# Performance work log

Hardware: AMD Instinct MI355X
Metric: run time of the kernel (lower is better)

Reference implementation:

```python
import jax, jax.numpy as jnp
import numpy as np

NUM_HEADS = 16
D_MODEL = 1024
DK = D_MODEL // NUM_HEADS


def setup_inputs() -> dict:
    key = jax.random.key(0)
    kH, kq, kk, kv, ko = jax.random.split(key, 5)
    scale = 0.02
    return {
        "H": jax.random.normal(kH, (4, 2048, D_MODEL), dtype=jnp.float32),
        "Wq": jax.random.normal(kq, (D_MODEL, D_MODEL), dtype=jnp.float32) * scale,
        "Wk": jax.random.normal(kk, (D_MODEL, D_MODEL), dtype=jnp.float32) * scale,
        "Wv": jax.random.normal(kv, (D_MODEL, D_MODEL), dtype=jnp.float32) * scale,
        "Wo": jax.random.normal(ko, (D_MODEL, D_MODEL), dtype=jnp.float32) * scale,
    }


def reference(H, Wq, Wk, Wv, Wo):
    b, T, d = H.shape
    n, dk = NUM_HEADS, DK
    # projections -> [b, n, T, dk]
    def split_heads(x):
        return x.reshape(b, T, n, dk).transpose(0, 2, 1, 3)
    Q = split_heads(H @ Wq)
    K = split_heads(H @ Wk)
    V = split_heads(H @ Wv)
    scores = jnp.einsum("bntd,bnsd->bnts", Q, K) / jnp.sqrt(jnp.float32(dk))
    causal = jnp.tril(jnp.ones((T, T), dtype=bool))
    scores = jnp.where(causal[None, None], scores, -jnp.inf)
    attn = jax.nn.softmax(scores, axis=-1)  # dropout rate 0 -> identity
    out = jnp.einsum("bnts,bnsd->bntd", attn, V)  # [b, n, T, dk]
    out = out.transpose(0, 2, 1, 3).reshape(b, T, n * dk)
    return out @ Wo
```

## Files before the change

### kernel.cpp

```cpp
#include <hip/hip_runtime.h>
#include <hip/hip_bf16.h>

#define T_SEQ 2048
#define DM 1024
#define DM2 2048
#define NH 16
#define DKH 64
#define NBATCH 4
#define MROWS (NBATCH*T_SEQ)

typedef __attribute__((ext_vector_type(8))) short bf16x8;
typedef __attribute__((ext_vector_type(4))) short bf16x4;
typedef __attribute__((ext_vector_type(4))) float f32x4;
typedef __attribute__((ext_vector_type(16))) float f32x16;
typedef __attribute__((ext_vector_type(4))) unsigned short u16x4;

#define NEG_INF (-__builtin_inff())

#if __has_builtin(__builtin_amdgcn_exp2f)
#define EXP2(x) __builtin_amdgcn_exp2f(x)
#else
#define EXP2(x) exp2f(x)
#endif

#define MFMA32(A,B,C) __builtin_amdgcn_mfma_f32_32x32x16_bf16(A,B,C,0,0,0)

static __device__ __forceinline__ unsigned short f2bf(float f){
  union { float f; unsigned u; } v; v.f = f;
  unsigned r = v.u + 0x7fffu + ((v.u >> 16) & 1u);
  return (unsigned short)(r >> 16);
}

static __device__ __forceinline__ unsigned short f2bfc(float f){
  union { __hip_bfloat16 h; unsigned short u; } cv;
  cv.h = __float2bfloat16(f);
  return cv.u;
}

static __device__ __forceinline__ void gload_lds16(const void* g, void* l){
  __builtin_amdgcn_global_load_lds(
      (const __attribute__((address_space(1))) void*)g,
      (__attribute__((address_space(3))) void*)l, 16, 0, 0);
}

__global__ __launch_bounds__(256) void convprep(
    const float* __restrict__ H,
    const float* __restrict__ W0, const float* __restrict__ W1,
    const float* __restrict__ W2, const float* __restrict__ W3,
    u16x4* __restrict__ Hb4,
    unsigned short* __restrict__ O0, unsigned short* __restrict__ O1,
    unsigned short* __restrict__ O2, unsigned short* __restrict__ O3)
{
  __shared__ float t[32][33];
  const int bid = blockIdx.x, tid = threadIdx.x;
  if (bid < 4096){
    const int z = bid >> 10, rem = bid & 1023;
    const int nx = (rem & 31)*32, kx = (rem >> 5)*32;
    const float* W = (z==0)?W0:(z==1)?W1:(z==2)?W2:W3;
    unsigned short* O = (z==0)?O0:(z==1)?O1:(z==2)?O2:O3;
    const float sc = (z==0) ? 0.18033688f : 1.0f;
    const int tx = tid & 31, ty = tid >> 5;
    #pragma unroll
    for (int i = 0; i < 4; ++i)
      t[ty + i*8][tx] = W[(size_t)(kx + ty + i*8)*DM + nx + tx];
    __syncthreads();
    #pragma unroll
    for (int i = 0; i < 4; ++i)
      O[(size_t)(nx + ty + i*8)*DM + kx + tx] = f2bf(t[tx][ty + i*8] * sc);
  } else {
    const int n4 = MROWS*DM/4;
    for (int i = (bid - 4096)*256 + tid; i < n4; i += 2048*256){
      float4 v = ((const float4*)H)[i];
      u16x4 o;
      o[0] = f2bf(v.x); o[1] = f2bf(v.y); o[2] = f2bf(v.z); o[3] = f2bf(v.w);
      Hb4[i] = o;
    }
  }
}

template<bool F32OUT>
static __device__ __forceinline__ void gemm_body(
    const unsigned short* __restrict__ A, const unsigned short* __restrict__ Bt,
    void* __restrict__ Cp, int N, int K, int m0, int n0,
    unsigned short* a_lds, unsigned short* b_lds)
{
  const int tid = threadIdx.x;
  const int w = tid >> 6, l = tid & 63;
  const int g = l >> 4, lr = l & 15;
  const int wr = w >> 1, wc = w & 1;
  f32x4 acc[4][4] = {};
  const int nk = K >> 6;
  for (int ks = 0; ks < nk; ++ks){
    __syncthreads();
    const int k0 = ks << 6;
    #pragma unroll
    for (int i = 0; i < 4; ++i){
      int c = (w*4 + i)*64 + l;
      int row = c >> 3;
      int gc = (c & 7) ^ (row & 7);
      gload_lds16(A + (size_t)(m0 + row)*K + (k0 + gc*8), &a_lds[c*8]);
    }
    #pragma unroll
    for (int i = 0; i < 4; ++i){
      int c = (w*4 + i)*64 + l;
      int row = c >> 3;
      int gc = (c & 7) ^ (row & 7);
      gload_lds16(Bt + (size_t)(n0 + row)*K + (k0 + gc*8), &b_lds[c*8]);
    }
    __syncthreads();
    #pragma unroll
    for (int kc = 0; kc < 2; ++kc){
      bf16x8 af[4], bf_[4];
      #pragma unroll
      for (int mt = 0; mt < 4; ++mt){
        int row = wr*64 + mt*16 + lr;
        int off = row*128 + ((kc*64 + g*16) ^ ((row & 7) << 4));
        af[mt] = *(const bf16x8*)((const char*)a_lds + off);
      }
      #pragma unroll
      for (int nt = 0; nt < 4; ++nt){
        int row = wc*64 + nt*16 + lr;
        int off = row*128 + ((kc*64 + g*16) ^ ((row & 7) << 4));
        bf_[nt] = *(const bf16x8*)((const char*)b_lds + off);
      }
      #pragma unroll
      for (int mt = 0; mt < 4; ++mt)
        #pragma unroll
        for (int nt = 0; nt < 4; ++nt)
          acc[mt][nt] = __builtin_amdgcn_mfma_f32_16x16x32_bf16(af[mt], bf_[nt], acc[mt][nt], 0, 0, 0);
    }
  }
  #pragma unroll
  for (int mt = 0; mt < 4; ++mt){
    #pragma unroll
    for (int nt = 0; nt < 4; ++nt){
      const int col = n0 + wc*64 + nt*16 + lr;
      #pragma unroll
      for (int r = 0; r < 4; ++r){
        const int row = m0 + wr*64 + mt*16 + 4*g + r;
        if (F32OUT) ((float*)Cp)[(size_t)row*N + col] = acc[mt][nt][r];
        else ((unsigned short*)Cp)[(size_t)row*N + col] = f2bf(acc[mt][nt][r]);
      }
    }
  }
}

__global__ __launch_bounds__(256) void gemm_qkv(
    const unsigned short* __restrict__ Hb, const unsigned short* __restrict__ Wqkt,
    unsigned short* __restrict__ QKb,
    const unsigned short* __restrict__ Wvt, unsigned short* __restrict__ Vtb)
{
  __shared__ __attribute__((aligned(16))) unsigned short a_lds[128*64];
  __shared__ __attribute__((aligned(16))) unsigned short b_lds[128*64];
  const int bid = blockIdx.x;
  const unsigned short *A, *Bt; unsigned short* Cp; int N, m0, n0;
  if (bid < 1024){
    A = Hb; Bt = Wqkt; Cp = QKb; N = DM2;
    m0 = (bid & 63)*128; n0 = (bid >> 6)*128;
  } else {
    const int t2 = bid - 1024;
    A = Wvt; Bt = Hb; Cp = Vtb; N = MROWS;
    m0 = (t2 & 7)*128; n0 = (t2 >> 3)*128;
  }
  gemm_body<false>(A, Bt, Cp, N, DM, m0, n0, a_lds, b_lds);
}

__global__ __launch_bounds__(256) void gemm_out(
    const unsigned short* __restrict__ Ab, const unsigned short* __restrict__ Wot,
    float* __restrict__ Out)
{
  __shared__ __attribute__((aligned(16))) unsigned short a_lds[128*64];
  __shared__ __attribute__((aligned(16))) unsigned short b_lds[128*64];
  gemm_body<true>(Ab, Wot, Out, DM, DM, blockIdx.x*128, blockIdx.y*128, a_lds, b_lds);
}

static __device__ __forceinline__ void half_softmax(
    f32x16& st0, f32x16& st1, float& m_run, float& l_run,
    f32x16& acc0, f32x16& acc1, bf16x8 (&pb)[4],
    int kvb, int qg, bool fullT)
{
  if (!fullT){
    #pragma unroll
    for (int r = 0; r < 16; ++r){
      const int kvo = (r & 3) + 4*((r >> 2) & 1) + 16*(r >> 3);
      st0[r] = (kvb + kvo      <= qg) ? st0[r] : NEG_INF;
      st1[r] = (kvb + 32 + kvo <= qg) ? st1[r] : NEG_INF;
    }
  }
  float m01[8];
  #pragma unroll
  for (int r = 0; r < 8; ++r)
    m01[r] = fmaxf(fmaxf(st0[2*r], st0[2*r+1]), fmaxf(st1[2*r], st1[2*r+1]));
  float tm = fmaxf(fmaxf(fmaxf(m01[0],m01[1]), fmaxf(m01[2],m01[3])),
                   fmaxf(fmaxf(m01[4],m01[5]), fmaxf(m01[6],m01[7])));
  float mm = m_run;
  if (!__all(tm - m_run <= 8.f)){
    float tg = fmaxf(tm, __shfl_xor(tm, 32));
    const float mn = fmaxf(m_run, tg);
    const float fac = EXP2(m_run - mn);
    l_run *= fac;
    #pragma unroll
    for (int r = 0; r < 16; ++r){ acc0[r] *= fac; acc1[r] *= fac; }
    m_run = mn; mm = mn;
  }
  float ps0 = 0.f, ps1 = 0.f, ps2 = 0.f, ps3 = 0.f;
  #pragma unroll
  for (int r = 0; r < 4; ++r){
    float e0 = EXP2(st0[4*r+0]-mm), e1 = EXP2(st0[4*r+1]-mm);
    float e2 = EXP2(st0[4*r+2]-mm), e3 = EXP2(st0[4*r+3]-mm);
    float f0 = EXP2(st1[4*r+0]-mm), f1 = EXP2(st1[4*r+1]-mm);
    float f2 = EXP2(st1[4*r+2]-mm), f3 = EXP2(st1[4*r+3]-mm);
    ps0 += e0 + f0; ps1 += e1 + f1; ps2 += e2 + f2; ps3 += e3 + f3;
    st0[4*r+0]=e0; st0[4*r+1]=e1; st0[4*r+2]=e2; st0[4*r+3]=e3;
    st1[4*r+0]=f0; st1[4*r+1]=f1; st1[4*r+2]=f2; st1[4*r+3]=f3;
  }
  l_run += (ps0 + ps1) + (ps2 + ps3);
  #pragma unroll
  for (int m = 0; m < 2; ++m){
    bf16x8 t0, t1;
    #pragma unroll
    for (int i = 0; i < 8; ++i){
      t0[i] = (short)f2bfc(st0[8*m+i]);
      t1[i] = (short)f2bfc(st1[8*m+i]);
    }
    pb[m] = t0; pb[2+m] = t1;
  }
}

__global__ __launch_bounds__(512, 2) void attn_kernel(const unsigned short* __restrict__ QK,
                                                      const unsigned short* __restrict__ Vt,
                                                      unsigned short* __restrict__ Og)
{
  __shared__ __attribute__((aligned(16))) unsigned short k_lds[2][128*64];
  __shared__ __attribute__((aligned(16))) unsigned short v_lds[2][64*128];
  const int tid = threadIdx.x;
  const int w = tid >> 6, l = tid & 63;
  const int h1 = l >> 5, lq = l & 31;
  const int L = blockIdx.x;
  const int xcd = L & 7, idx = L >> 3;
  const int bh = xcd*8 + (idx & 7);
  const int pair = idx >> 3;
  const int b = bh >> 4, h = bh & 15;
  const size_t baseK = (size_t)(b*T_SEQ)*DM2 + 1024 + h*DKH;
  const size_t baseV = (size_t)(h*DKH)*MROWS + (size_t)b*T_SEQ;

  const int cA = tid, cB = tid + 512;
  const int krA = cA >> 3, krB = cB >> 3;
  const int kiA = (cA & 7) ^ (krA & 7), kiB = (cB & 7) ^ (krB & 7);
  const int kvA = 32*(krA >> 5) + 16*((krA >> 4) & 1) + 8*((krA >> 2) & 1) + 4*((krA >> 3) & 1) + (krA & 3);
  const int kvB = 32*(krB >> 5) + 16*((krB >> 4) & 1) + 8*((krB >> 2) & 1) + 4*((krB >> 3) & 1) + (krB & 3);
  const int vrA = cA >> 4, vgA = (cA & 15) ^ (vrA & 15);
  const int vrB = cB >> 4, vgB = (cB & 15) ^ (vrB & 15);

  auto STAGE = [&](int jt, int buf){
    const int j0s = jt * 128;
    gload_lds16(QK + baseK + (size_t)(j0s + kvA)*DM2 + kiA*8, &k_lds[buf][cA*8]);
    gload_lds16(QK + baseK + (size_t)(j0s + kvB)*DM2 + kiB*8, &k_lds[buf][cB*8]);
    gload_lds16(Vt + baseV + (size_t)vrA*MROWS + j0s + vgA*8, &v_lds[buf][cA*8]);
    gload_lds16(Vt + baseV + (size_t)vrB*MROWS + j0s + vgB*8, &v_lds[buf][cB*8]);
  };

#define ROUND(JT, CUR) do{                                                        \
    const int jt_ = (JT);                                                         \
    if (jt_ + 1 < ntiles) STAGE(jt_ + 1, (CUR)^1);                                \
    const int j0_ = jt_ * 128;                                                    \
    _Pragma("unroll")                                                             \
    for (int h2 = 0; h2 < 2; ++h2){                                               \
      if (j0_ + 64*h2 <= qhi){                                                    \
        f32x16 st0 = {}, st1 = {};                                                \
        __builtin_amdgcn_s_setprio(1);                                            \
        _Pragma("unroll")                                                         \
        for (int s = 0; s < 4; ++s){                                              \
          const int r0_ = 64*h2 + lq, r1_ = r0_ + 32;                             \
          bf16x8 kf0 = *(const bf16x8*)((const char*)k_lds[CUR] + r0_*128 + (((2*s + h1) ^ (r0_ & 7)) << 4)); \
          bf16x8 kf1 = *(const bf16x8*)((const char*)k_lds[CUR] + r1_*128 + (((2*s + h1) ^ (r1_ & 7)) << 4)); \
          st0 = MFMA32(kf0, qf[s], st0);                                          \
          st1 = MFMA32(kf1, qf[s], st1);                                          \
        }                                                                         \
        __builtin_amdgcn_s_setprio(0);                                            \
        bf16x8 pb[4];                                                             \
        half_softmax(st0, st1, m_run, l_run, acc0, acc1, pb,                      \
                     j0_ + 64*h2 + 8*h1, qg, (j0_ + 64*h2 + 63) <= qlo);          \
        __builtin_amdgcn_s_setprio(1);                                            \
        _Pragma("unroll")                                                         \
        for (int jl = 0; jl < 4; ++jl){                                           \
          const int vr0 = lq, vr1 = 32 + lq;                                      \
          bf16x8 vf0 = *(const bf16x8*)((const char*)v_lds[CUR] + vr0*256 + (((2*(4*h2 + jl) + h1) ^ (vr0 & 15)) << 4)); \
          bf16x8 vf1 = *(const bf16x8*)((const char*)v_lds[CUR] + vr1*256 + (((2*(4*h2 + jl) + h1) ^ (vr1 & 15)) << 4)); \
          acc0 = MFMA32(vf0, pb[jl], acc0);                                       \
          acc1 = MFMA32(vf1, pb[jl], acc1);                                       \
        }                                                                         \
        __builtin_amdgcn_s_setprio(0);                                            \
      }                                                                           \
    }                                                                             \
    __syncthreads();                                                              \
  } while(0)

  #pragma unroll 1
  for (int seg = 0; seg < 2; ++seg){
    const int qblk = seg ? pair : (7 - pair);
    const int q0 = qblk * 256;
    const int qlo = q0 + 32*w;
    const int qhi = qlo + 31;
    const int qg = qlo + lq;
    const size_t rowQ = (size_t)(b*T_SEQ + qg)*DM2 + h*DKH;
    bf16x8 qf[4];
    #pragma unroll
    for (int s = 0; s < 4; ++s)
      qf[s] = *(const bf16x8*)(QK + rowQ + 16*s + 8*h1);
    float m_run = NEG_INF, l_run = 0.f;
    f32x16 acc0 = {}, acc1 = {};
    const int ntiles = 2*qblk + 2;

    STAGE(0, 0);
    __syncthreads();

    #pragma unroll 1
    for (int jt = 0; jt < ntiles; jt += 2){
      ROUND(jt, 0);
      ROUND(jt + 1, 1);
    }

    const float ls = l_run + __shfl_xor(l_run, 32);
    const float inv = 1.f / ls;
    const size_t rowO = (size_t)(b*T_SEQ + qg)*DM + h*DKH;
    #pragma unroll
    for (int d = 0; d < 2; ++d){
      const f32x16& A = d ? acc1 : acc0;
      #pragma unroll
      for (int bb = 0; bb < 4; ++bb){
        unsigned u0 = (unsigned)f2bfc(A[4*bb+0]*inv) | ((unsigned)f2bfc(A[4*bb+1]*inv) << 16);
        unsigned u1 = (unsigned)f2bfc(A[4*bb+2]*inv) | ((unsigned)f2bfc(A[4*bb+3]*inv) << 16);
        uint2 uv; uv.x = u0; uv.y = u1;
        *(uint2*)(Og + rowO + 32*d + 8*bb + 4*h1) = uv;
      }
    }
  }
#undef ROUND
}

extern "C" void kernel_launch(void* const* d_in, const int* in_sizes, int n_in,
                              void* d_out, int out_size, void* d_ws, size_t ws_size,
                              hipStream_t stream)
{
  (void)in_sizes; (void)n_in; (void)out_size; (void)ws_size;
  const float* H  = (const float*)d_in[0];
  const float* Wq = (const float*)d_in[1];
  const float* Wk = (const float*)d_in[2];
  const float* Wv = (const float*)d_in[3];
  const float* Wo = (const float*)d_in[4];
  char* ws = (char*)d_ws;
  unsigned short* Hb   = (unsigned short*)(ws);
  unsigned short* Wqkt = (unsigned short*)(ws + 16777216);
  unsigned short* Wkt  = (unsigned short*)(ws + 18874368);
  unsigned short* Wvt  = (unsigned short*)(ws + 20971520);
  unsigned short* Wot  = (unsigned short*)(ws + 23068672);
  unsigned short* QKb  = (unsigned short*)(ws + 25165824);
  unsigned short* Vtb  = (unsigned short*)(ws + 58720256);
  unsigned short* Ab   = (unsigned short*)(ws + 75497472);

  convprep<<<6144, 256, 0, stream>>>(H, Wq, Wk, Wv, Wo,
                                     (u16x4*)Hb, Wqkt, Wkt, Wvt, Wot);
  gemm_qkv<<<1536, 256, 0, stream>>>(Hb, Wqkt, QKb, Wvt, Vtb);
  attn_kernel<<<dim3(256), 512, 0, stream>>>(QKb, Vtb, Ab);
  gemm_out<<<dim3(64,8), 256, 0, stream>>>(Ab, Wot, (float*)d_out);
}
```

Baseline: 154.2 us.

## Add 256x256 double-buffered 8-wave GEMM for QK projection, split V GEMM

Replaces the combined QKV projection launch with a dedicated 256x256-tile, 512-thread kernel for the Q/K projection. It double-buffers swizzled LDS tiles via direct global-to-LDS loads and interleaves LDS reads, async loads and MFMA clusters under explicit barriers, waitcnts and priority hints. The V-transpose projection moves to its own launch using the old 128x128 body. The intent is higher MFMA utilization and more reuse per loaded tile. In exchange it uses 128KB of LDS per block and a fragile hand-tuned schedule, and it adds one extra kernel launch.

```diff
diff --git a/kernel.cpp b/kernel.cpp
--- a/kernel.cpp
+++ b/kernel.cpp
@@ -78,6 +78,130 @@
   }
 }
 
+__global__ __launch_bounds__(512, 2) void gemm_qk8(
+    const unsigned short* __restrict__ A, const unsigned short* __restrict__ Bt,
+    unsigned short* __restrict__ C)
+{
+  __shared__ __attribute__((aligned(16))) unsigned short lds[2][32768];
+  const int tid = threadIdx.x;
+  const int w = tid >> 6, l = tid & 63;
+  const int g = l >> 4, lr = l & 15;
+  const int wr = w >> 2, wc = w & 3;
+  const int bid = blockIdx.x;
+  const int m0 = (bid & 31) * 256, n0 = (bid >> 5) * 256;
+
+  const int c0 = (w*2)*64 + l, c1 = (w*2+1)*64 + l;
+  const int r0 = c0 >> 3, gc0 = (c0 & 7) ^ (r0 & 7);
+  const int r1 = c1 >> 3, gc1 = (c1 & 7) ^ (r1 & 7);
+
+  auto STA = [&](int h, int t, int buf){
+    gload_lds16(A + (size_t)(m0 + h*128 + r0)*DM + t*64 + gc0*8,
+                (char*)lds + buf*65536 + h*16384 + c0*16);
+    gload_lds16(A + (size_t)(m0 + h*128 + r1)*DM + t*64 + gc1*8,
+                (char*)lds + buf*65536 + h*16384 + c1*16);
+  };
+  auto STB = [&](int h, int t, int buf){
+    gload_lds16(Bt + (size_t)(n0 + h*128 + r0)*DM + t*64 + gc0*8,
+                (char*)lds + buf*65536 + 32768 + h*16384 + c0*16);
+    gload_lds16(Bt + (size_t)(n0 + h*128 + r1)*DM + t*64 + gc1*8,
+                (char*)lds + buf*65536 + 32768 + h*16384 + c1*16);
+  };
+
+  f32x4 acc[8][4] = {};
+  bf16x8 af[8], bf[8];
+
+  STB(0,0,0); STB(1,0,0); STA(0,0,0); STA(1,0,0);
+  STB(0,1,1); STB(1,1,1); STA(0,1,1); STA(1,1,1);
+  asm volatile("s_waitcnt vmcnt(8)");
+  __builtin_amdgcn_s_barrier();
+
+#define RDA(BUF, MH) do{ _Pragma("unroll") for (int mi=0;mi<4;++mi){            \
+    const int ra = ((MH)*4+mi)*16 + lr;                                         \
+    _Pragma("unroll") for (int kc=0;kc<2;++kc)                                  \
+      af[mi*2+kc] = *(const bf16x8*)((const char*)lds + (BUF)*65536             \
+        + wr*16384 + ra*128 + ((kc*64+g*16) ^ ((ra&7)<<4))); } }while(0)
+#define RDB(BUF, NHI) do{ _Pragma("unroll") for (int ni=0;ni<2;++ni){           \
+    const int nt = (NHI)*2+ni; const int rb = (wc&1)*64 + nt*16 + lr;           \
+    _Pragma("unroll") for (int kc=0;kc<2;++kc)                                  \
+      bf[nt*2+kc] = *(const bf16x8*)((const char*)lds + (BUF)*65536 + 32768     \
+        + (wc>>1)*16384 + rb*128 + ((kc*64+g*16) ^ ((rb&7)<<4))); } }while(0)
+#define MF(MH, NHI) do{ _Pragma("unroll") for (int mi=0;mi<4;++mi)              \
+    _Pragma("unroll") for (int ni=0;ni<2;++ni)                                  \
+    _Pragma("unroll") for (int kc=0;kc<2;++kc)                                  \
+      acc[(MH)*4+mi][(NHI)*2+ni] = __builtin_amdgcn_mfma_f32_16x16x32_bf16(     \
+        af[mi*2+kc], bf[((NHI)*2+ni)*2+kc], acc[(MH)*4+mi][(NHI)*2+ni],0,0,0); }while(0)
+#define WAITL0 do{ asm volatile("s_waitcnt lgkmcnt(0)");                        \
+    __builtin_amdgcn_sched_barrier(0); }while(0)
+
+  #pragma unroll 1
+  for (int i = 0; i < 8; ++i){
+    const int t1 = 2*i+1, t2 = 2*i+2, t3 = 2*i+3;
+    RDA(0,0); RDB(0,0);
+    if (i > 0) STA(0, t1, 1);
+    asm volatile("s_waitcnt lgkmcnt(8)");
+    __builtin_amdgcn_s_barrier();
+    WAITL0;
+    __builtin_amdgcn_s_setprio(1); MF(0,0); __builtin_amdgcn_s_setprio(0);
+    __builtin_amdgcn_s_barrier();
+    RDB(0,1);
+    if (i > 0) STA(1, t1, 1);
+    __builtin_amdgcn_s_barrier();
+    WAITL0;
+    __builtin_amdgcn_s_setprio(1); MF(0,1); __builtin_amdgcn_s_setprio(0);
+    __builtin_amdgcn_s_barrier();
+    RDA(0,1);
+    if (i < 7) STB(0, t2, 0);
+    __builtin_amdgcn_s_barrier();
+    WAITL0;
+    __builtin_amdgcn_s_setprio(1); MF(1,1); __builtin_amdgcn_s_setprio(0);
+    __builtin_amdgcn_s_barrier();
+    if (i < 7) STB(1, t2, 0);
+    __builtin_amdgcn_s_setprio(1); MF(1,0); __builtin_amdgcn_s_setprio(0);
+    if (i < 7) asm volatile("s_waitcnt vmcnt(4)");
+    else       asm volatile("s_waitcnt vmcnt(0)");
+    __builtin_amdgcn_s_barrier();
+    RDA(1,0); RDB(1,0);
+    if (i < 7) STA(0, t2, 0);
+    asm volatile("s_waitcnt lgkmcnt(8)");
+    __builtin_amdgcn_s_barrier();
+    WAITL0;
+    __builtin_amdgcn_s_setprio(1); MF(0,0); __builtin_amdgcn_s_setprio(0);
+    __builtin_amdgcn_s_barrier();
+    RDB(1,1);
+    if (i < 7) STA(1, t2, 0);
+    __builtin_amdgcn_s_barrier();
+    WAITL0;
+    __builtin_amdgcn_s_setprio(1); MF(0,1); __builtin_amdgcn_s_setprio(0);
+    __builtin_amdgcn_s_barrier();
+    RDA(1,1);
+    if (i < 7) STB(0, t3, 1);
+    __builtin_amdgcn_s_barrier();
+    WAITL0;
+    __builtin_amdgcn_s_setprio(1); MF(1,1); __builtin_amdgcn_s_setprio(0);
+    __builtin_amdgcn_s_barrier();
+    if (i < 7) STB(1, t3, 1);
+    __builtin_amdgcn_s_setprio(1); MF(1,0); __builtin_amdgcn_s_setprio(0);
+    asm volatile("s_waitcnt vmcnt(4)");
+    __builtin_amdgcn_s_barrier();
+  }
+#undef RDA
+#undef RDB
+#undef MF
+#undef WAITL0
+
+  #pragma unroll
+  for (int mt = 0; mt < 8; ++mt){
+    const int row_b = m0 + wr*128 + mt*16 + 4*g;
+    #pragma unroll
+    for (int nt = 0; nt < 4; ++nt){
+      const int col = n0 + wc*64 + nt*16 + lr;
+      #pragma unroll
+      for (int r = 0; r < 4; ++r)
+        C[(size_t)(row_b + r)*DM2 + col] = f2bf(acc[mt][nt][r]);
+    }
+  }
+}
+
 template<bool F32OUT>
 static __device__ __forceinline__ void gemm_body(
     const unsigned short* __restrict__ A, const unsigned short* __restrict__ Bt,
@@ -145,24 +269,13 @@
   }
 }
 
-__global__ __launch_bounds__(256) void gemm_qkv(
-    const unsigned short* __restrict__ Hb, const unsigned short* __restrict__ Wqkt,
-    unsigned short* __restrict__ QKb,
-    const unsigned short* __restrict__ Wvt, unsigned short* __restrict__ Vtb)
+__global__ __launch_bounds__(256) void gemm_vt(
+    const unsigned short* __restrict__ Wvt, const unsigned short* __restrict__ Hb,
+    unsigned short* __restrict__ Vtb)
 {
   __shared__ __attribute__((aligned(16))) unsigned short a_lds[128*64];
   __shared__ __attribute__((aligned(16))) unsigned short b_lds[128*64];
-  const int bid = blockIdx.x;
-  const unsigned short *A, *Bt; unsigned short* Cp; int N, m0, n0;
-  if (bid < 1024){
-    A = Hb; Bt = Wqkt; Cp = QKb; N = DM2;
-    m0 = (bid & 63)*128; n0 = (bid >> 6)*128;
-  } else {
-    const int t2 = bid - 1024;
-    A = Wvt; Bt = Hb; Cp = Vtb; N = MROWS;
-    m0 = (t2 & 7)*128; n0 = (t2 >> 3)*128;
-  }
-  gemm_body<false>(A, Bt, Cp, N, DM, m0, n0, a_lds, b_lds);
+  gemm_body<false>(Wvt, Hb, Vtb, MROWS, DM, blockIdx.x*128, blockIdx.y*128, a_lds, b_lds);
 }
 
 __global__ __launch_bounds__(256) void gemm_out(
@@ -326,11 +439,11 @@
     const size_t rowO = (size_t)(b*T_SEQ + qg)*DM + h*DKH;
     #pragma unroll
     for (int d = 0; d < 2; ++d){
-      const f32x16& A = d ? acc1 : acc0;
+      const f32x16& Aq = d ? acc1 : acc0;
       #pragma unroll
       for (int bb = 0; bb < 4; ++bb){
-        unsigned u0 = (unsigned)f2bfc(A[4*bb+0]*inv) | ((unsigned)f2bfc(A[4*bb+1]*inv) << 16);
-        unsigned u1 = (unsigned)f2bfc(A[4*bb+2]*inv) | ((unsigned)f2bfc(A[4*bb+3]*inv) << 16);
+        unsigned u0 = (unsigned)f2bfc(Aq[4*bb+0]*inv) | ((unsigned)f2bfc(Aq[4*bb+1]*inv) << 16);
+        unsigned u1 = (unsigned)f2bfc(Aq[4*bb+2]*inv) | ((unsigned)f2bfc(Aq[4*bb+3]*inv) << 16);
         uint2 uv; uv.x = u0; uv.y = u1;
         *(uint2*)(Og + rowO + 32*d + 8*bb + 4*h1) = uv;
       }
@@ -361,7 +474,8 @@
 
   convprep<<<6144, 256, 0, stream>>>(H, Wq, Wk, Wv, Wo,
                                      (u16x4*)Hb, Wqkt, Wkt, Wvt, Wot);
-  gemm_qkv<<<1536, 256, 0, stream>>>(Hb, Wqkt, QKb, Wvt, Vtb);
+  gemm_qk8<<<256, 512, 0, stream>>>(Hb, Wqkt, QKb);
+  gemm_vt<<<dim3(8,64), 256, 0, stream>>>(Wvt, Hb, Vtb);
   attn_kernel<<<dim3(256), 512, 0, stream>>>(QKb, Vtb, Ab);
   gemm_out<<<dim3(64,8), 256, 0, stream>>>(Ab, Wot, (float*)d_out);
 }
```

Result: no change. 152.5 us (median of 3 runs) (-1.1%).
